# Performance work log

Measured on AMD Instinct MI355X. Metric: run time of the kernel, lower is better.

## Reference

```python
import jax, jax.numpy as jnp
import numpy as np

EPS = 1e-12  # F.normalize default eps


def _normalize(x):
    # F.normalize(x): x / max(||x||_2 over dim=1, eps)
    n = jnp.sqrt(jnp.sum(x * x, axis=1, keepdims=True))
    return x / jnp.maximum(n, EPS)


def _layer_loss(t, s, n):
    d = (_normalize(t) - _normalize(s)) ** 2
    # np.percentile(., 99.9) with linear interpolation == jnp.quantile(., 0.999);
    # torch version detaches (cpu numpy), so stop_gradient matches semantics.
    dhard = jax.lax.stop_gradient(jnp.quantile(d.reshape(-1), 0.999))
    mask = d >= dhard
    cnt = jnp.sum(mask).astype(d.dtype)
    hard_mean = jnp.sum(jnp.where(mask, d, 0.0)) / cnt
    return hard_mean + jnp.mean(n * n)


def setup_inputs() -> dict:
    key = jax.random.key(0)
    shapes = {
        't1': (16, 64, 128, 128), 's1': (16, 64, 128, 128), 'n1': (16, 64, 128, 128),
        't2': (16, 128, 64, 64),  's2': (16, 128, 64, 64),  'n2': (16, 128, 64, 64),
        't3': (16, 256, 32, 32),  's3': (16, 256, 32, 32),  'n3': (16, 256, 32, 32),
    }
    ks = jax.random.split(key, len(shapes))
    return {name: jax.random.normal(k, shp, dtype=jnp.float32)
            for k, (name, shp) in zip(ks, shapes.items())}


def reference(t1, s1, n1, t2, s2, n2, t3, s3, n3):
    losses = jnp.stack([
        _layer_loss(t1, s1, n1),
        _layer_loss(t2, s2, n2),
        _layer_loss(t3, s3, n3),
    ])
    return jnp.sum(losses)
```

## Files before the change

kernel.cpp:

```cpp
#include <hip/hip_runtime.h>

#define NBINS 2304
#define BINBASE 2048
#define ACC_OFF (3 * NBINS)

typedef float    f4v __attribute__((ext_vector_type(4)));
typedef _Float16 h4v __attribute__((ext_vector_type(4)));

template<int C, int HWSHIFT, int PSHIFT, int LAYER>
__device__ __forceinline__ void hist_layer(
    const float* __restrict__ t, const float* __restrict__ s, const float* __restrict__ n,
    int lb, unsigned int* __restrict__ ws_u, float* __restrict__ ws_f,
    unsigned int* cnt_sh, float* ov_sh, float* inv_sh)
{
    const int HW  = 1 << HWSHIFT;
    const int P   = 1 << PSHIFT;
    const int NPQ = P >> 2;
    const int G   = 1024 >> PSHIFT;
    const int tid = threadIdx.x;
    const int w   = tid >> 6;
    const int l   = tid & 63;
    const int pq  = l & (NPQ - 1);
    const int cs  = l >> (PSHIFT - 2);

    const int p0 = lb << PSHIFT;
    const int b  = p0 >> HWSHIFT;
    const int q  = p0 & (HW - 1);
    const int c0 = w * (C / 4) + cs * 16;
    const size_t base = ((size_t)(b * C + c0) << HWSHIFT) + q + 4 * pq;

    const float* tp = t + base;
    const float* sp = s + base;
    const float* np = n + base;

    #pragma unroll
    for (int i = tid; i < NBINS / 4; i += 256)
        ((uint4*)cnt_sh)[i] = make_uint4(0u, 0u, 0u, 0u);

    h4v th[16], sh[16];
    f4v accT = {0.f,0.f,0.f,0.f}, accS = {0.f,0.f,0.f,0.f};
    float aN = 0.f;

    #pragma unroll
    for (int k0 = 0; k0 < 16; k0 += 4) {
        f4v tt[4], ss[4], nn[4];
        #pragma unroll
        for (int u = 0; u < 4; ++u) {
            const size_t o = (size_t)(k0 + u) << HWSHIFT;
            tt[u] = *(const f4v*)(tp + o);
            ss[u] = *(const f4v*)(sp + o);
            nn[u] = __builtin_nontemporal_load((const f4v*)(np + o));
        }
        #pragma unroll
        for (int u = 0; u < 4; ++u) {
            accT += tt[u] * tt[u];
            accS += ss[u] * ss[u];
            aN += nn[u].x*nn[u].x + nn[u].y*nn[u].y + nn[u].z*nn[u].z + nn[u].w*nn[u].w;
            th[k0+u] = (h4v){(_Float16)tt[u].x, (_Float16)tt[u].y,
                             (_Float16)tt[u].z, (_Float16)tt[u].w};
            sh[k0+u] = (h4v){(_Float16)ss[u].x, (_Float16)ss[u].y,
                             (_Float16)ss[u].z, (_Float16)ss[u].w};
        }
    }

    float* ovT = ov_sh;
    float* ovS = ov_sh + 1024;
    float* ovN = ov_sh + 2048;
    const int g = (w * (64 / NPQ)) + cs;
    ((f4v*)ovT)[g * NPQ + pq] = accT;
    ((f4v*)ovS)[g * NPQ + pq] = accS;
    #pragma unroll
    for (int o = 32; o > 0; o >>= 1) aN += __shfl_down(aN, o, 64);
    if (l == 0) ovN[w] = aN;
    __syncthreads();

    if (tid < P) {
        float nT = 0.f, nS = 0.f;
        #pragma unroll
        for (int gg = 0; gg < G; ++gg) { nT += ovT[gg * P + tid]; nS += ovS[gg * P + tid]; }
        inv_sh[tid]     = 1.0f / fmaxf(sqrtf(nT), 1e-12f);
        inv_sh[P + tid] = 1.0f / fmaxf(sqrtf(nS), 1e-12f);
    }
    if (tid == 0)
        atomicAdd(&ws_f[ACC_OFF + LAYER], ovN[0] + ovN[1] + ovN[2] + ovN[3]);
    __syncthreads();

    __builtin_amdgcn_s_setprio(1);
    f4v iT = ((const f4v*)inv_sh)[pq];
    f4v iS = ((const f4v*)(inv_sh + P))[pq];
    #pragma unroll
    for (int k = 0; k < 16; ++k) {
        f4v tv = {(float)th[k].x, (float)th[k].y, (float)th[k].z, (float)th[k].w};
        f4v sv = {(float)sh[k].x, (float)sh[k].y, (float)sh[k].z, (float)sh[k].w};
        f4v a  = tv * iT - sv * iS;
        f4v d  = a * a;
        int b0 = min(max((int)(__float_as_uint(d.x) >> 18) - BINBASE, 0), NBINS - 1);
        int b1 = min(max((int)(__float_as_uint(d.y) >> 18) - BINBASE, 0), NBINS - 1);
        int b2 = min(max((int)(__float_as_uint(d.z) >> 18) - BINBASE, 0), NBINS - 1);
        int b3 = min(max((int)(__float_as_uint(d.w) >> 18) - BINBASE, 0), NBINS - 1);
        atomicAdd(&cnt_sh[b0], 1u);
        atomicAdd(&cnt_sh[b1], 1u);
        atomicAdd(&cnt_sh[b2], 1u);
        atomicAdd(&cnt_sh[b3], 1u);
    }
    __syncthreads();

    unsigned int* gc = ws_u + LAYER * NBINS;
    #pragma unroll
    for (int i = tid; i < NBINS; i += 256) {
        unsigned c = cnt_sh[i];
        if (c) atomicAdd(&gc[i], c);
    }
    __builtin_amdgcn_s_setprio(0);
}

__global__ __launch_bounds__(256, 3) void stfpm_hist(
    const float* __restrict__ t0, const float* __restrict__ s0, const float* __restrict__ n0,
    const float* __restrict__ t1, const float* __restrict__ s1, const float* __restrict__ n1,
    const float* __restrict__ t2, const float* __restrict__ s2, const float* __restrict__ n2,
    unsigned int* __restrict__ ws_u, float* __restrict__ ws_f)
{
    __shared__ __align__(16) unsigned int cnt_sh[NBINS];
    __shared__ __align__(16) float ov_sh[2052];
    __shared__ __align__(16) float inv_sh[512];
    const int bid = blockIdx.x;
    if (bid < 256)
        hist_layer<256, 10, 6, 2>(t2, s2, n2, bid,       ws_u, ws_f, cnt_sh, ov_sh, inv_sh);
    else if (bid < 768)
        hist_layer<128, 12, 7, 1>(t1, s1, n1, bid - 256, ws_u, ws_f, cnt_sh, ov_sh, inv_sh);
    else
        hist_layer<64,  14, 8, 0>(t0, s0, n0, bid - 768, ws_u, ws_f, cnt_sh, ov_sh, inv_sh);
}

__device__ __forceinline__ float bin_lo(int b) {
    return __uint_as_float((unsigned)(b + BINBASE) << 18);
}
__device__ __forceinline__ float bin_mid(int b) {
    return 0.5f * (bin_lo(b) + bin_lo(b + 1));
}

__global__ __launch_bounds__(256) void stfpm_finalize(
    const unsigned int* __restrict__ ws_u, const float* __restrict__ ws_f,
    float* __restrict__ out)
{
    __shared__ unsigned int cchunk[256];
    __shared__ float        schunk[256];
    const int tid = threadIdx.x;

    const int   targets[3] = {16778, 8389, 4195};
    const float Ns[3]      = {16777216.f, 8388608.f, 4194304.f};
    const int   CHUNK = NBINS / 256;

    float total = 0.f;
    for (int layer = 0; layer < 3; ++layer) {
        const unsigned int* gc = ws_u + layer * NBINS;
        unsigned int c = 0; float sv = 0.f;
        const int b0 = tid * CHUNK;
        for (int i = 0; i < CHUNK; ++i) {
            unsigned cc = gc[b0 + i];
            c += cc;
            if (cc) sv += (float)cc * bin_mid(b0 + i);
        }
        __syncthreads();
        cchunk[tid] = c; schunk[tid] = sv;
        __syncthreads();
        if (tid == 0) {
            const int target = targets[layer];
            long long cum = 0; float sAbove = 0.f;
            int ch = 255;
            while (ch >= 0 && cum + (long long)cchunk[ch] < target) {
                cum += cchunk[ch]; sAbove += schunk[ch]; --ch;
            }
            int bin = ch * CHUNK + CHUNK - 1;
            while (bin >= ch * CHUNK && cum + (long long)gc[bin] < target) {
                unsigned cc = gc[bin];
                cum += cc; sAbove += (float)cc * bin_mid(bin); --bin;
            }
            unsigned cb = gc[bin];
            int j = target - (int)cum;
            float lo = bin_lo(bin), hi = bin_lo(bin + 1);
            float wd = hi - lo;
            float f  = (float)j / (float)cb;
            float topmean = hi - f * wd * 0.5f;
            topmean = fminf(fmaxf(topmean, lo), hi);
            float hard   = (sAbove + topmean * (float)j) / (float)target;
            float n2mean = ws_f[ACC_OFF + layer] / Ns[layer];
            total += hard + n2mean;
        }
        __syncthreads();
    }
    if (tid == 0) out[0] = total;
}

extern "C" void kernel_launch(void* const* d_in, const int* in_sizes, int n_in,
                              void* d_out, int out_size, void* d_ws, size_t ws_size,
                              hipStream_t stream)
{
    const float* t0 = (const float*)d_in[0];
    const float* s0 = (const float*)d_in[1];
    const float* n0 = (const float*)d_in[2];
    const float* t1 = (const float*)d_in[3];
    const float* s1 = (const float*)d_in[4];
    const float* n1 = (const float*)d_in[5];
    const float* t2 = (const float*)d_in[6];
    const float* s2 = (const float*)d_in[7];
    const float* n2 = (const float*)d_in[8];

    hipMemsetAsync(d_ws, 0, (size_t)(ACC_OFF + 8) * 4, stream);

    stfpm_hist<<<1792, 256, 0, stream>>>(t0, s0, n0, t1, s1, n1, t2, s2, n2,
                                         (unsigned int*)d_ws, (float*)d_ws);
    stfpm_finalize<<<1, 256, 0, stream>>>((const unsigned int*)d_ws,
                                          (const float*)d_ws, (float*)d_out);
}
```

Baseline: 81.30 us.

## Split noise sum-of-squares into separate interleaved blocks from t/s histogram blocks

Moves the sum of squares over n out of the histogram blocks into dedicated lightweight blocks. These are interleaved one in three with the t/s blocks, and the grid grows from 1792 to 2688 blocks. The histogram blocks get less register pressure and fewer loads, and the n streaming blocks can run alongside them to balance memory traffic. In exchange there are more block launches and more atomic adds to the per-layer accumulator, one per wavefront instead of one per block.

```diff
diff --git a/kernel.cpp b/kernel.cpp
--- a/kernel.cpp
+++ b/kernel.cpp
@@ -8,9 +8,9 @@
 typedef _Float16 h4v __attribute__((ext_vector_type(4)));
 
 template<int C, int HWSHIFT, int PSHIFT, int LAYER>
-__device__ __forceinline__ void hist_layer(
-    const float* __restrict__ t, const float* __restrict__ s, const float* __restrict__ n,
-    int lb, unsigned int* __restrict__ ws_u, float* __restrict__ ws_f,
+__device__ __forceinline__ void ts_block(
+    const float* __restrict__ t, const float* __restrict__ s,
+    int lb, unsigned int* __restrict__ ws_u,
     unsigned int* cnt_sh, float* ov_sh, float* inv_sh)
 {
     const int HW  = 1 << HWSHIFT;
@@ -31,7 +31,6 @@
 
     const float* tp = t + base;
     const float* sp = s + base;
-    const float* np = n + base;
 
     #pragma unroll
     for (int i = tid; i < NBINS / 4; i += 256)
@@ -39,23 +38,20 @@
 
     h4v th[16], sh[16];
     f4v accT = {0.f,0.f,0.f,0.f}, accS = {0.f,0.f,0.f,0.f};
-    float aN = 0.f;
 
     #pragma unroll
     for (int k0 = 0; k0 < 16; k0 += 4) {
-        f4v tt[4], ss[4], nn[4];
+        f4v tt[4], ss[4];
         #pragma unroll
         for (int u = 0; u < 4; ++u) {
             const size_t o = (size_t)(k0 + u) << HWSHIFT;
             tt[u] = *(const f4v*)(tp + o);
             ss[u] = *(const f4v*)(sp + o);
-            nn[u] = __builtin_nontemporal_load((const f4v*)(np + o));
         }
         #pragma unroll
         for (int u = 0; u < 4; ++u) {
             accT += tt[u] * tt[u];
             accS += ss[u] * ss[u];
-            aN += nn[u].x*nn[u].x + nn[u].y*nn[u].y + nn[u].z*nn[u].z + nn[u].w*nn[u].w;
             th[k0+u] = (h4v){(_Float16)tt[u].x, (_Float16)tt[u].y,
                              (_Float16)tt[u].z, (_Float16)tt[u].w};
             sh[k0+u] = (h4v){(_Float16)ss[u].x, (_Float16)ss[u].y,
@@ -65,13 +61,9 @@
 
     float* ovT = ov_sh;
     float* ovS = ov_sh + 1024;
-    float* ovN = ov_sh + 2048;
     const int g = (w * (64 / NPQ)) + cs;
     ((f4v*)ovT)[g * NPQ + pq] = accT;
     ((f4v*)ovS)[g * NPQ + pq] = accS;
-    #pragma unroll
-    for (int o = 32; o > 0; o >>= 1) aN += __shfl_down(aN, o, 64);
-    if (l == 0) ovN[w] = aN;
     __syncthreads();
 
     if (tid < P) {
@@ -81,8 +73,6 @@
         inv_sh[tid]     = 1.0f / fmaxf(sqrtf(nT), 1e-12f);
         inv_sh[P + tid] = 1.0f / fmaxf(sqrtf(nS), 1e-12f);
     }
-    if (tid == 0)
-        atomicAdd(&ws_f[ACC_OFF + LAYER], ovN[0] + ovN[1] + ovN[2] + ovN[3]);
     __syncthreads();
 
     __builtin_amdgcn_s_setprio(1);
@@ -114,6 +104,21 @@
     __builtin_amdgcn_s_setprio(0);
 }
 
+__device__ __forceinline__ void n_block(
+    const float* __restrict__ n, int layer, int nb, float* __restrict__ ws_f)
+{
+    const f4v* p = (const f4v*)n + ((size_t)nb << 13) + threadIdx.x;
+    float a = 0.f;
+    #pragma unroll 8
+    for (int i = 0; i < 32; ++i) {
+        f4v v = __builtin_nontemporal_load(p + (size_t)i * 256);
+        a += v.x*v.x + v.y*v.y + v.z*v.z + v.w*v.w;
+    }
+    #pragma unroll
+    for (int o = 32; o > 0; o >>= 1) a += __shfl_down(a, o, 64);
+    if ((threadIdx.x & 63) == 0) atomicAdd(&ws_f[ACC_OFF + layer], a);
+}
+
 __global__ __launch_bounds__(256, 3) void stfpm_hist(
     const float* __restrict__ t0, const float* __restrict__ s0, const float* __restrict__ n0,
     const float* __restrict__ t1, const float* __restrict__ s1, const float* __restrict__ n1,
@@ -121,15 +126,24 @@
     unsigned int* __restrict__ ws_u, float* __restrict__ ws_f)
 {
     __shared__ __align__(16) unsigned int cnt_sh[NBINS];
-    __shared__ __align__(16) float ov_sh[2052];
+    __shared__ __align__(16) float ov_sh[2048];
     __shared__ __align__(16) float inv_sh[512];
     const int bid = blockIdx.x;
-    if (bid < 256)
-        hist_layer<256, 10, 6, 2>(t2, s2, n2, bid,       ws_u, ws_f, cnt_sh, ov_sh, inv_sh);
-    else if (bid < 768)
-        hist_layer<128, 12, 7, 1>(t1, s1, n1, bid - 256, ws_u, ws_f, cnt_sh, ov_sh, inv_sh);
+    const int g   = bid / 3;
+    const int r   = bid - g * 3;
+    if (r == 2) {
+        if (g < 128)      n_block(n2, 2, g,       ws_f);
+        else if (g < 384) n_block(n1, 1, g - 128, ws_f);
+        else              n_block(n0, 0, g - 384, ws_f);
+        return;
+    }
+    const int ts = g * 2 + r;
+    if (ts < 256)
+        ts_block<256, 10, 6, 2>(t2, s2, ts,       ws_u, cnt_sh, ov_sh, inv_sh);
+    else if (ts < 768)
+        ts_block<128, 12, 7, 1>(t1, s1, ts - 256, ws_u, cnt_sh, ov_sh, inv_sh);
     else
-        hist_layer<64,  14, 8, 0>(t0, s0, n0, bid - 768, ws_u, ws_f, cnt_sh, ov_sh, inv_sh);
+        ts_block<64,  14, 8, 0>(t0, s0, ts - 768, ws_u, cnt_sh, ov_sh, inv_sh);
 }
 
 __device__ __forceinline__ float bin_lo(int b) {
@@ -208,7 +222,7 @@
 
     hipMemsetAsync(d_ws, 0, (size_t)(ACC_OFF + 8) * 4, stream);
 
-    stfpm_hist<<<1792, 256, 0, stream>>>(t0, s0, n0, t1, s1, n1, t2, s2, n2,
+    stfpm_hist<<<2688, 256, 0, stream>>>(t0, s0, n0, t1, s1, n1, t2, s2, n2,
                                          (unsigned int*)d_ws, (float*)d_ws);
     stfpm_finalize<<<1, 256, 0, stream>>>((const unsigned int*)d_ws,
                                           (const float*)d_ws, (float*)d_out);
```

After: 93.73 us. 15.3% more time.
